# Kernel tuning notes

Hardware: AMD Instinct MI355X
Metric: run time of the kernel (lower is better)

## Reference

```python
import jax, jax.numpy as jnp
from jax import lax
import numpy as np

RANK = 4
C_IN = 32
C_OUT = 64
H, W = 128, 256
L1 = (H + 2, W + 2)      # conv k=3, pad=2, stride=1 -> H+2
L2 = (L1[0] + 2, L1[1] + 2)
EPS = 1e-5


def setup_inputs() -> dict:
    key = jax.random.key(0)
    ks = jax.random.split(key, 12)
    s = lambda k, shp: jax.random.normal(k, shp, dtype=jnp.float32) * 0.05
    inp = {
        "x": jax.random.normal(ks[0], (16, C_IN, H, W), dtype=jnp.float32),
        # layer 1: rank basis kernels, bias, outer combining-weight logits
        "w1": s(ks[1], (RANK, C_OUT, C_IN, 3, 3)),
        "b1": jnp.zeros((C_OUT,), jnp.float32),
        "a1h": s(ks[2], (RANK, L1[0])),
        "a1w": s(ks[3], (RANK, L1[1])),
        "g1": jnp.ones((C_OUT,), jnp.float32),
        "be1": jnp.zeros((C_OUT,), jnp.float32),
        # layer 2
        "w2": s(ks[4], (RANK, C_OUT, C_OUT, 3, 3)),
        "b2": jnp.zeros((C_OUT,), jnp.float32),
        "a2h": s(ks[5], (RANK, L2[0])),
        "a2w": s(ks[6], (RANK, L2[1])),
        "g2": jnp.ones((C_OUT,), jnp.float32),
        "be2": jnp.zeros((C_OUT,), jnp.float32),
    }
    return inp


def _combining_weights(ah, aw):
    # outer sum of row/col logits, softmax over rank -> [rank, Lh, Lw]
    return jax.nn.softmax(ah[:, :, None] + aw[:, None, :], axis=0)


def _lrlc(x, w, b, cw):
    # x: [B, Cin, H, W]; w: [rank, Cout, Cin, 3, 3]; cw: [rank, H', W']
    rank, co, ci, kh, kw = w.shape
    y = lax.conv_general_dilated(
        x, w.reshape(rank * co, ci, kh, kw),
        window_strides=(1, 1), padding=[(2, 2), (2, 2)],
        dimension_numbers=("NCHW", "OIHW", "NCHW"))
    B, _, Ho, Wo = y.shape
    y = y.reshape(B, rank, co, Ho, Wo)
    return jnp.einsum("brohw,rhw->bohw", y, cw) + b[None, :, None, None]


def _bn_relu(x, g, be):
    # training-mode BatchNorm2d (batch stats, biased variance) + ReLU
    mean = jnp.mean(x, axis=(0, 2, 3), keepdims=True)
    var = jnp.var(x, axis=(0, 2, 3), keepdims=True)
    xn = (x - mean) * lax.rsqrt(var + EPS)
    return jax.nn.relu(xn * g[None, :, None, None] + be[None, :, None, None])


def _maxpool3(x):
    return lax.reduce_window(x, -jnp.inf, lax.max,
                             (1, 1, 3, 3), (1, 1, 3, 3), "VALID")


def reference(x, w1, b1, a1h, a1w, g1, be1, w2, b2, a2h, a2w, g2, be2):
    cw1 = _combining_weights(a1h, a1w)
    h = _lrlc(x, w1, b1, cw1)
    h = _bn_relu(h, g1, be1)
    cw2 = _combining_weights(a2h, a2w)
    h = _lrlc(h, w2, b2, cw2)
    h = _bn_relu(h, g2, be2)
    return _maxpool3(h)
```

## Files before the change

kernel.cpp:

```cpp
#include <hip/hip_runtime.h>
#include <hip/hip_bf16.h>
#include <math.h>

#define COUT 64
#define EPS  1e-5f

typedef __hip_bfloat16 bf16;
typedef short  short8  __attribute__((ext_vector_type(8)));
typedef short  short4v __attribute__((ext_vector_type(4)));
typedef float  floatx4 __attribute__((ext_vector_type(4)));

__device__ __forceinline__ short bf16_bits(float f) {
    union { __hip_bfloat16 h; short s; } u;
    u.h = __float2bfloat16(f);
    return u.s;
}
__device__ __forceinline__ float bits_to_f32(short s) {
    union { __hip_bfloat16 h; short s; } u;
    u.s = s;
    return __bfloat162float(u.h);
}

#define NV1   33800
#define NV2   34584
#define XPAD_PLANE  (132*260)
#define H1_PLANE    (134*262)
#define H2_PLANE    (132*260)
#define NPOS1 (16*130*258)
#define NPOS2 (16*132*260)

__global__ void zero_f_kernel(float* __restrict__ p, int n) {
    int i = blockIdx.x*blockDim.x + threadIdx.x;
    if (i < n) p[i] = 0.f;
}
__global__ void zero4_kernel(uint4* __restrict__ p, long n4) {
    long i = (long)blockIdx.x*blockDim.x + threadIdx.x;
    for (; i < n4; i += (long)gridDim.x*blockDim.x) p[i] = make_uint4(0,0,0,0);
}

__global__ void cwv_kernel(const float* __restrict__ ah, const float* __restrict__ aw,
                           float* __restrict__ cwv, int Nv, int Wv, int Lh, int Lw) {
    int idx = blockIdx.x*blockDim.x + threadIdx.x;
    if (idx >= Nv) return;
    int oh = idx / Wv, ow = idx - oh*Wv;
    if (ow > Lw-1) ow = Lw-1;
    float v0 = ah[0*Lh+oh] + aw[0*Lw+ow];
    float v1 = ah[1*Lh+oh] + aw[1*Lw+ow];
    float v2 = ah[2*Lh+oh] + aw[2*Lw+ow];
    float v3 = ah[3*Lh+oh] + aw[3*Lw+ow];
    float m = fmaxf(fmaxf(v0,v1), fmaxf(v2,v3));
    v0 = __expf(v0-m); v1 = __expf(v1-m); v2 = __expf(v2-m); v3 = __expf(v3-m);
    float inv = 1.f/(v0+v1+v2+v3);
    cwv[0*(size_t)Nv+idx] = v0*inv; cwv[1*(size_t)Nv+idx] = v1*inv;
    cwv[2*(size_t)Nv+idx] = v2*inv; cwv[3*(size_t)Nv+idx] = v3*inv;
}

template<int CIN_, int NSLICES>
__global__ void pack_kernel(const float* __restrict__ w, short* __restrict__ Apk) {
    int gid = blockIdx.x*256 + threadIdx.x;
    if (gid >= NSLICES*1024) return;
    int l = gid & 63, t = (gid >> 6) & 15, s = gid >> 10;
    int m = t*16 + (l & 15);
    int r = m >> 6, co = m & 63;
    int kbase = s*32 + ((l >> 4) << 3);
    short8 v;
    #pragma unroll
    for (int j = 0; j < 8; ++j) {
        int k = kbase + j;
        int tap = k / CIN_, ci = k % CIN_;
        float f = w[(((size_t)(r*COUT + co))*CIN_ + ci)*9 + tap];
        v[j] = bf16_bits(f);
    }
    *reinterpret_cast<short8*>(Apk + (size_t)gid*8) = v;
}

__global__ void xpad_kernel(const float* __restrict__ x, short* __restrict__ xp) {
    int row = blockIdx.x;
    int b = row / 132, ih = row - b*132;
    int ci = threadIdx.x & 31, iw0 = threadIdx.x >> 5;
    for (int iw = iw0; iw < 260; iw += 8) {
        float v = 0.f;
        if (ih >= 2 && ih < 130 && iw >= 2 && iw < 258)
            v = x[(((size_t)b*32 + ci)*128 + (ih-2))*256 + (iw-2)];
        xp[((size_t)row*260 + iw)*32 + ci] = bf16_bits(v);
    }
}

template<int CIN_, int NSLICES>
__launch_bounds__(256, 2)
__global__ void lrlc_conv(const short* __restrict__ Bpl, const short* __restrict__ Apk,
                          const float* __restrict__ cwv, const float* __restrict__ bias,
                          short* __restrict__ Out,
                          int Wv, int Hout, int Wreal, int Nv, int inPlanePos,
                          int outW, int outPlanePos, int outPad) {
    const int tid  = threadIdx.x;
    const int w    = tid >> 6, l = tid & 63;
    const int quad = l >> 4, l15 = l & 15;
    const int b    = blockIdx.y;
    const int n0   = blockIdx.x * 64;

    __shared__ float cwS[4*64];
    {
        int r = tid >> 6, nn = tid & 63;
        int n = n0 + nn; if (n > Nv-1) n = Nv-1;
        cwS[r*64 + nn] = cwv[(size_t)r*Nv + n];
    }
    __syncthreads();

    const short* Bb = Bpl + (size_t)b*inPlanePos*CIN_;
    int bOff[4];
    #pragma unroll
    for (int j = 0; j < 4; ++j) bOff[j] = (n0 + j*16 + l15)*CIN_ + quad*8;
    const short* Aw = Apk + (size_t)(w*64 + l)*8;

    floatx4 acc[4][4];
    #pragma unroll
    for (int i = 0; i < 4; ++i)
        #pragma unroll
        for (int j = 0; j < 4; ++j)
            acc[i][j] = (floatx4){0.f,0.f,0.f,0.f};

    for (int s = 0; s < NSLICES; ++s) {
        const int tap = (CIN_ == 32) ? s : (s >> 1);
        const int cb  = (CIN_ == 32) ? 0 : ((s & 1) << 5);
        const int koff = ((tap/3)*Wv + (tap%3))*CIN_ + cb;
        short8 bfr[4], afr[4];
        #pragma unroll
        for (int j = 0; j < 4; ++j)
            bfr[j] = *reinterpret_cast<const short8*>(Bb + bOff[j] + koff);
        #pragma unroll
        for (int i = 0; i < 4; ++i)
            afr[i] = *reinterpret_cast<const short8*>(Aw + (size_t)(s*16 + i*4)*512);
        #pragma unroll
        for (int i = 0; i < 4; ++i)
            #pragma unroll
            for (int j = 0; j < 4; ++j)
                acc[i][j] = __builtin_amdgcn_mfma_f32_16x16x32_bf16(afr[i], bfr[j], acc[i][j], 0, 0, 0);
    }

    const int co_base = w*16 + quad*4;
    float bs[4];
    #pragma unroll
    for (int rg = 0; rg < 4; ++rg) bs[rg] = bias[co_base + rg];
    #pragma unroll
    for (int j = 0; j < 4; ++j) {
        int nl = j*16 + l15;
        int n  = n0 + nl;
        int oh = n / Wv, ow = n - oh*Wv;
        if (ow >= Wreal || oh >= Hout) continue;
        float c0 = cwS[nl], c1 = cwS[64+nl], c2 = cwS[128+nl], c3 = cwS[192+nl];
        short4v pk;
        #pragma unroll
        for (int rg = 0; rg < 4; ++rg) {
            float v = acc[0][j][rg]*c0 + acc[1][j][rg]*c1
                    + acc[2][j][rg]*c2 + acc[3][j][rg]*c3 + bs[rg];
            pk[rg] = bf16_bits(v);
        }
        size_t op = ((size_t)b*outPlanePos + (size_t)(oh + outPad)*outW + (ow + outPad))*(size_t)COUT + co_base;
        *reinterpret_cast<short4v*>(Out + op) = pk;
    }
}

__global__ void stats_nhwc(const short* __restrict__ h, float* __restrict__ sum,
                           float* __restrict__ sq, int npos, int Wreal, int Hreal,
                           int rowW, int planePos, int pad) {
    int c = threadIdx.x & 63, sub = threadIdx.x >> 6;
    float s = 0.f, s2 = 0.f;
    for (long p = blockIdx.x*4 + sub; p < npos; p += (long)gridDim.x*4) {
        int ow = (int)(p % Wreal); long t2 = p / Wreal;
        int oh = (int)(t2 % Hreal); int b = (int)(t2 / Hreal);
        float v = bits_to_f32(h[((size_t)b*planePos + (size_t)(oh+pad)*rowW + ow + pad)*64 + c]);
        s += v; s2 = fmaf(v, v, s2);
    }
    __shared__ float ls[4][64], ls2[4][64];
    ls[sub][c] = s; ls2[sub][c] = s2;
    __syncthreads();
    if (threadIdx.x < 64) {
        float ts  = ls[0][c]+ls[1][c]+ls[2][c]+ls[3][c];
        float ts2 = ls2[0][c]+ls2[1][c]+ls2[2][c]+ls2[3][c];
        atomicAdd(&sum[c], ts);
        atomicAdd(&sq[c], ts2);
    }
}

__global__ void finalize_kernel(const float* __restrict__ sum, const float* __restrict__ sumsq,
                                const float* __restrict__ g, const float* __restrict__ be,
                                float* __restrict__ A, float* __restrict__ Bc, float cnt) {
    int c = threadIdx.x;
    if (c >= COUT) return;
    float mean = sum[c]/cnt;
    float var  = sumsq[c]/cnt - mean*mean;
    float inv  = rsqrtf(var + EPS);
    float a = g[c]*inv;
    A[c]  = a;
    Bc[c] = fmaf(-mean, a, be[c]);
}

__global__ void bnrelu_nhwc(short* __restrict__ h, const float* __restrict__ A,
                            const float* __restrict__ Bc, int npos, int Wreal, int Hreal,
                            int rowW, int planePos, int pad) {
    __shared__ float sA[64], sB[64];
    if (threadIdx.x < 64) { sA[threadIdx.x] = A[threadIdx.x]; sB[threadIdx.x] = Bc[threadIdx.x]; }
    __syncthreads();
    long g = (long)blockIdx.x*256 + threadIdx.x;
    if (g >= (long)npos*16) return;
    int cg = (int)(g & 15); long p = g >> 4;
    int ow = (int)(p % Wreal); long t2 = p / Wreal;
    int oh = (int)(t2 % Hreal); int b = (int)(t2 / Hreal);
    size_t base = ((size_t)b*planePos + (size_t)(oh+pad)*rowW + ow + pad)*64 + cg*4;
    short4v d = *reinterpret_cast<short4v*>(h + base);
    #pragma unroll
    for (int q = 0; q < 4; ++q) {
        float v = bits_to_f32(d[q]);
        int c = cg*4 + q;
        v = fmaxf(fmaf(v, sA[c], sB[c]), 0.f);
        d[q] = bf16_bits(v);
    }
    *reinterpret_cast<short4v*>(h + base) = d;
}

__global__ void maxpool_nhwc(const short* __restrict__ h2, const float* __restrict__ A,
                             const float* __restrict__ Bc, float* __restrict__ out) {
    int idx = blockIdx.x*blockDim.x + threadIdx.x;
    const int total = 16*64*44*86;
    if (idx >= total) return;
    int pw = idx % 86; int t = idx / 86;
    int ph = t % 44;   t /= 44;
    int c  = t % 64;   int b = t / 64;
    float a = A[c], bc = Bc[c];
    float m = 0.f;
    #pragma unroll
    for (int i = 0; i < 3; ++i) {
        size_t rbase = ((size_t)(b*132 + ph*3 + i)*260 + pw*3)*64 + c;
        #pragma unroll
        for (int j = 0; j < 3; ++j) {
            float v = fmaf(bits_to_f32(h2[rbase + (size_t)j*64]), a, bc);
            m = fmaxf(m, v);
        }
    }
    out[idx] = m;
}

extern "C" void kernel_launch(void* const* d_in, const int* in_sizes, int n_in,
                              void* d_out, int out_size, void* d_ws, size_t ws_size,
                              hipStream_t stream) {
    const float* x   = (const float*)d_in[0];
    const float* w1  = (const float*)d_in[1];
    const float* b1  = (const float*)d_in[2];
    const float* a1h = (const float*)d_in[3];
    const float* a1w = (const float*)d_in[4];
    const float* g1  = (const float*)d_in[5];
    const float* be1 = (const float*)d_in[6];
    const float* w2  = (const float*)d_in[7];
    const float* b2  = (const float*)d_in[8];
    const float* a2h = (const float*)d_in[9];
    const float* a2w = (const float*)d_in[10];
    const float* g2  = (const float*)d_in[11];
    const float* be2 = (const float*)d_in[12];
    float* out = (float*)d_out;

    char* ws = (char*)d_ws;
    float* stats = (float*)ws;
    float* sum1 = stats;       float* sq1 = stats + 64;
    float* A1   = stats + 128; float* Bc1 = stats + 192;
    float* sum2 = stats + 256; float* sq2 = stats + 320;
    float* A2   = stats + 384; float* Bc2 = stats + 448;
    float* cw1v = (float*)(ws + 2048);
    float* cw2v = cw1v + 4*NV1;
    short* Apk1 = (short*)(cw2v + 4*NV2);
    short* Apk2 = Apk1 + 73728;
    short* h1pad = Apk2 + 147456;
    short* xpad  = h1pad + (size_t)16*H1_PLANE*64 + 4096;
    short* h2    = xpad;

    zero_f_kernel<<<2, 256, 0, stream>>>(stats, 512);
    {
        long n4 = ((size_t)16*H1_PLANE*64 + 4096) * 2 / 16;
        zero4_kernel<<<4096, 256, 0, stream>>>((uint4*)h1pad, n4);
    }
    cwv_kernel<<<(NV1+255)/256, 256, 0, stream>>>(a1h, a1w, cw1v, NV1, 260, 130, 258);
    cwv_kernel<<<(NV2+255)/256, 256, 0, stream>>>(a2h, a2w, cw2v, NV2, 262, 132, 260);
    pack_kernel<32, 9><<<(9*1024+255)/256, 256, 0, stream>>>(w1, Apk1);
    pack_kernel<64,18><<<(18*1024+255)/256, 256, 0, stream>>>(w2, Apk2);
    xpad_kernel<<<16*132, 256, 0, stream>>>(x, xpad);

    lrlc_conv<32, 9><<<dim3((NV1+63)/64, 16), 256, 0, stream>>>(
        xpad, Apk1, cw1v, b1, h1pad,
        260, 130, 258, NV1, XPAD_PLANE,
        262, H1_PLANE, 2);
    stats_nhwc<<<256, 256, 0, stream>>>(h1pad, sum1, sq1, NPOS1, 258, 130, 262, H1_PLANE, 2);
    finalize_kernel<<<1, 64, 0, stream>>>(sum1, sq1, g1, be1, A1, Bc1, (float)NPOS1);
    bnrelu_nhwc<<<((long)NPOS1*16 + 255)/256, 256, 0, stream>>>(h1pad, A1, Bc1, NPOS1, 258, 130, 262, H1_PLANE, 2);

    lrlc_conv<64,18><<<dim3((NV2+63)/64, 16), 256, 0, stream>>>(
        h1pad, Apk2, cw2v, b2, h2,
        262, 132, 260, NV2, H1_PLANE,
        260, H2_PLANE, 0);
    stats_nhwc<<<256, 256, 0, stream>>>(h2, sum2, sq2, NPOS2, 260, 132, 260, H2_PLANE, 0);
    finalize_kernel<<<1, 64, 0, stream>>>(sum2, sq2, g2, be2, A2, Bc2, (float)NPOS2);

    maxpool_nhwc<<<(16*64*44*86 + 255)/256, 256, 0, stream>>>(h2, A2, Bc2, out);
}
```

Baseline: 1.349 ms.

## Fuse BN stats into conv epilogue, widen conv tile, vectorize bnrelu and maxpool

New measurement: 1.186 ms. -12.1%, faster.

```diff
diff --git a/kernel.cpp b/kernel.cpp
--- a/kernel.cpp
+++ b/kernel.cpp
@@ -68,8 +68,7 @@
     for (int j = 0; j < 8; ++j) {
         int k = kbase + j;
         int tap = k / CIN_, ci = k % CIN_;
-        float f = w[(((size_t)(r*COUT + co))*CIN_ + ci)*9 + tap];
-        v[j] = bf16_bits(f);
+        v[j] = bf16_bits(w[(((size_t)(r*COUT + co))*CIN_ + ci)*9 + tap]);
     }
     *reinterpret_cast<short8*>(Apk + (size_t)gid*8) = v;
 }
@@ -90,43 +89,44 @@
 __launch_bounds__(256, 2)
 __global__ void lrlc_conv(const short* __restrict__ Bpl, const short* __restrict__ Apk,
                           const float* __restrict__ cwv, const float* __restrict__ bias,
-                          short* __restrict__ Out,
+                          short* __restrict__ Out, float* __restrict__ sum, float* __restrict__ sq,
                           int Wv, int Hout, int Wreal, int Nv, int inPlanePos,
                           int outW, int outPlanePos, int outPad) {
     const int tid  = threadIdx.x;
     const int w    = tid >> 6, l = tid & 63;
     const int quad = l >> 4, l15 = l & 15;
     const int b    = blockIdx.y;
-    const int n0   = blockIdx.x * 64;
-
-    __shared__ float cwS[4*64];
-    {
-        int r = tid >> 6, nn = tid & 63;
+    const int n0   = blockIdx.x * 128;
+
+    __shared__ float cwS[4*128];
+    for (int t = tid; t < 512; t += 256) {
+        int r = t >> 7, nn = t & 127;
         int n = n0 + nn; if (n > Nv-1) n = Nv-1;
-        cwS[r*64 + nn] = cwv[(size_t)r*Nv + n];
+        cwS[t] = cwv[(size_t)r*Nv + n];
     }
     __syncthreads();
 
     const short* Bb = Bpl + (size_t)b*inPlanePos*CIN_;
-    int bOff[4];
-    #pragma unroll
-    for (int j = 0; j < 4; ++j) bOff[j] = (n0 + j*16 + l15)*CIN_ + quad*8;
+    int bOff[8];
+    #pragma unroll
+    for (int j = 0; j < 8; ++j) bOff[j] = (n0 + j*16 + l15)*CIN_ + quad*8;
     const short* Aw = Apk + (size_t)(w*64 + l)*8;
 
-    floatx4 acc[4][4];
+    floatx4 acc[4][8];
     #pragma unroll
     for (int i = 0; i < 4; ++i)
         #pragma unroll
-        for (int j = 0; j < 4; ++j)
+        for (int j = 0; j < 8; ++j)
             acc[i][j] = (floatx4){0.f,0.f,0.f,0.f};
 
+    #pragma unroll
     for (int s = 0; s < NSLICES; ++s) {
         const int tap = (CIN_ == 32) ? s : (s >> 1);
         const int cb  = (CIN_ == 32) ? 0 : ((s & 1) << 5);
         const int koff = ((tap/3)*Wv + (tap%3))*CIN_ + cb;
-        short8 bfr[4], afr[4];
-        #pragma unroll
-        for (int j = 0; j < 4; ++j)
+        short8 bfr[8], afr[4];
+        #pragma unroll
+        for (int j = 0; j < 8; ++j)
             bfr[j] = *reinterpret_cast<const short8*>(Bb + bOff[j] + koff);
         #pragma unroll
         for (int i = 0; i < 4; ++i)
@@ -134,7 +134,7 @@
         #pragma unroll
         for (int i = 0; i < 4; ++i)
             #pragma unroll
-            for (int j = 0; j < 4; ++j)
+            for (int j = 0; j < 8; ++j)
                 acc[i][j] = __builtin_amdgcn_mfma_f32_16x16x32_bf16(afr[i], bfr[j], acc[i][j], 0, 0, 0);
     }
 
@@ -142,44 +142,41 @@
     float bs[4];
     #pragma unroll
     for (int rg = 0; rg < 4; ++rg) bs[rg] = bias[co_base + rg];
-    #pragma unroll
-    for (int j = 0; j < 4; ++j) {
+    float st[4] = {0.f,0.f,0.f,0.f}, st2[4] = {0.f,0.f,0.f,0.f};
+    #pragma unroll
+    for (int j = 0; j < 8; ++j) {
         int nl = j*16 + l15;
         int n  = n0 + nl;
         int oh = n / Wv, ow = n - oh*Wv;
-        if (ow >= Wreal || oh >= Hout) continue;
-        float c0 = cwS[nl], c1 = cwS[64+nl], c2 = cwS[128+nl], c3 = cwS[192+nl];
+        bool valid = (ow < Wreal) && (oh < Hout);
+        float c0 = cwS[nl], c1 = cwS[128+nl], c2 = cwS[256+nl], c3 = cwS[384+nl];
         short4v pk;
         #pragma unroll
         for (int rg = 0; rg < 4; ++rg) {
             float v = acc[0][j][rg]*c0 + acc[1][j][rg]*c1
                     + acc[2][j][rg]*c2 + acc[3][j][rg]*c3 + bs[rg];
+            if (valid) { st[rg] += v; st2[rg] = fmaf(v, v, st2[rg]); }
             pk[rg] = bf16_bits(v);
         }
-        size_t op = ((size_t)b*outPlanePos + (size_t)(oh + outPad)*outW + (ow + outPad))*(size_t)COUT + co_base;
-        *reinterpret_cast<short4v*>(Out + op) = pk;
-    }
-}
-
-__global__ void stats_nhwc(const short* __restrict__ h, float* __restrict__ sum,
-                           float* __restrict__ sq, int npos, int Wreal, int Hreal,
-                           int rowW, int planePos, int pad) {
-    int c = threadIdx.x & 63, sub = threadIdx.x >> 6;
-    float s = 0.f, s2 = 0.f;
-    for (long p = blockIdx.x*4 + sub; p < npos; p += (long)gridDim.x*4) {
-        int ow = (int)(p % Wreal); long t2 = p / Wreal;
-        int oh = (int)(t2 % Hreal); int b = (int)(t2 / Hreal);
-        float v = bits_to_f32(h[((size_t)b*planePos + (size_t)(oh+pad)*rowW + ow + pad)*64 + c]);
-        s += v; s2 = fmaf(v, v, s2);
-    }
-    __shared__ float ls[4][64], ls2[4][64];
-    ls[sub][c] = s; ls2[sub][c] = s2;
-    __syncthreads();
-    if (threadIdx.x < 64) {
-        float ts  = ls[0][c]+ls[1][c]+ls[2][c]+ls[3][c];
-        float ts2 = ls2[0][c]+ls2[1][c]+ls2[2][c]+ls2[3][c];
-        atomicAdd(&sum[c], ts);
-        atomicAdd(&sq[c], ts2);
+        if (valid) {
+            size_t op = ((size_t)b*outPlanePos + (size_t)(oh + outPad)*outW + (ow + outPad))*(size_t)COUT + co_base;
+            *reinterpret_cast<short4v*>(Out + op) = pk;
+        }
+    }
+    #pragma unroll
+    for (int m = 1; m < 16; m <<= 1) {
+        #pragma unroll
+        for (int rg = 0; rg < 4; ++rg) {
+            st[rg]  += __shfl_xor(st[rg],  m, 16);
+            st2[rg] += __shfl_xor(st2[rg], m, 16);
+        }
+    }
+    if (l15 == 0) {
+        #pragma unroll
+        for (int rg = 0; rg < 4; ++rg) {
+            atomicAdd(&sum[co_base+rg], st[rg]);
+            atomicAdd(&sq[co_base+rg],  st2[rg]);
+        }
     }
 }
 
@@ -196,49 +193,57 @@
     Bc[c] = fmaf(-mean, a, be[c]);
 }
 
-__global__ void bnrelu_nhwc(short* __restrict__ h, const float* __restrict__ A,
-                            const float* __restrict__ Bc, int npos, int Wreal, int Hreal,
-                            int rowW, int planePos, int pad) {
+__global__ void bnrelu_rows(short* __restrict__ h, const float* __restrict__ A,
+                            const float* __restrict__ Bc) {
     __shared__ float sA[64], sB[64];
     if (threadIdx.x < 64) { sA[threadIdx.x] = A[threadIdx.x]; sB[threadIdx.x] = Bc[threadIdx.x]; }
     __syncthreads();
-    long g = (long)blockIdx.x*256 + threadIdx.x;
-    if (g >= (long)npos*16) return;
-    int cg = (int)(g & 15); long p = g >> 4;
-    int ow = (int)(p % Wreal); long t2 = p / Wreal;
-    int oh = (int)(t2 % Hreal); int b = (int)(t2 / Hreal);
-    size_t base = ((size_t)b*planePos + (size_t)(oh+pad)*rowW + ow + pad)*64 + cg*4;
-    short4v d = *reinterpret_cast<short4v*>(h + base);
-    #pragma unroll
-    for (int q = 0; q < 4; ++q) {
-        float v = bits_to_f32(d[q]);
-        int c = cg*4 + q;
-        v = fmaxf(fmaf(v, sA[c], sB[c]), 0.f);
-        d[q] = bf16_bits(v);
-    }
-    *reinterpret_cast<short4v*>(h + base) = d;
-}
-
-__global__ void maxpool_nhwc(const short* __restrict__ h2, const float* __restrict__ A,
+    int row = blockIdx.x;
+    int b = row / 130, oh = row - b*130;
+    short* base = h + ((size_t)(b*134 + oh + 2)*262 + 2)*64;
+    const int nvec = 258*64/8;
+    for (int it = threadIdx.x; it < nvec; it += 256) {
+        short8 d = *reinterpret_cast<short8*>(base + it*8);
+        int c0 = (it*8) & 63;
+        #pragma unroll
+        for (int q = 0; q < 8; ++q) {
+            float v = bits_to_f32(d[q]);
+            int c = c0 + q;
+            v = fmaxf(fmaf(v, sA[c], sB[c]), 0.f);
+            d[q] = bf16_bits(v);
+        }
+        *reinterpret_cast<short8*>(base + it*8) = d;
+    }
+}
+
+__global__ void maxpool_rows(const short* __restrict__ h2, const float* __restrict__ A,
                              const float* __restrict__ Bc, float* __restrict__ out) {
-    int idx = blockIdx.x*blockDim.x + threadIdx.x;
-    const int total = 16*64*44*86;
-    if (idx >= total) return;
-    int pw = idx % 86; int t = idx / 86;
-    int ph = t % 44;   t /= 44;
-    int c  = t % 64;   int b = t / 64;
-    float a = A[c], bc = Bc[c];
-    float m = 0.f;
-    #pragma unroll
-    for (int i = 0; i < 3; ++i) {
-        size_t rbase = ((size_t)(b*132 + ph*3 + i)*260 + pw*3)*64 + c;
-        #pragma unroll
-        for (int j = 0; j < 3; ++j) {
-            float v = fmaf(bits_to_f32(h2[rbase + (size_t)j*64]), a, bc);
-            m = fmaxf(m, v);
-        }
-    }
-    out[idx] = m;
+    __shared__ float sA[64], sB[64];
+    if (threadIdx.x < 64) { sA[threadIdx.x] = A[threadIdx.x]; sB[threadIdx.x] = Bc[threadIdx.x]; }
+    __syncthreads();
+    int row = blockIdx.x;
+    int b = row / 44, ph = row - b*44;
+    for (int item = threadIdx.x; item < 86*16; item += 256) {
+        int cg = item & 15, pw = item >> 4;
+        float m[4] = {0.f,0.f,0.f,0.f};
+        #pragma unroll
+        for (int i = 0; i < 3; ++i) {
+            const short* rp = h2 + ((size_t)(b*132 + ph*3 + i)*260 + pw*3)*64 + cg*4;
+            #pragma unroll
+            for (int j = 0; j < 3; ++j) {
+                short4v d = *reinterpret_cast<const short4v*>(rp + j*64);
+                #pragma unroll
+                for (int q = 0; q < 4; ++q) {
+                    int c = cg*4 + q;
+                    float v = fmaf(bits_to_f32(d[q]), sA[c], sB[c]);
+                    m[q] = fmaxf(m[q], v);
+                }
+            }
+        }
+        #pragma unroll
+        for (int q = 0; q < 4; ++q)
+            out[((size_t)(b*64 + cg*4 + q)*44 + ph)*86 + pw] = m[q];
+    }
 }
 
 extern "C" void kernel_launch(void* const* d_in, const int* in_sizes, int n_in,
@@ -284,20 +289,16 @@
     pack_kernel<64,18><<<(18*1024+255)/256, 256, 0, stream>>>(w2, Apk2);
     xpad_kernel<<<16*132, 256, 0, stream>>>(x, xpad);
 
-    lrlc_conv<32, 9><<<dim3((NV1+63)/64, 16), 256, 0, stream>>>(
-        xpad, Apk1, cw1v, b1, h1pad,
-        260, 130, 258, NV1, XPAD_PLANE,
-        262, H1_PLANE, 2);
-    stats_nhwc<<<256, 256, 0, stream>>>(h1pad, sum1, sq1, NPOS1, 258, 130, 262, H1_PLANE, 2);
+    lrlc_conv<32, 9><<<dim3((NV1+127)/128, 16), 256, 0, stream>>>(
+        xpad, Apk1, cw1v, b1, h1pad, sum1, sq1,
+        260, 130, 258, NV1, XPAD_PLANE, 262, H1_PLANE, 2);
     finalize_kernel<<<1, 64, 0, stream>>>(sum1, sq1, g1, be1, A1, Bc1, (float)NPOS1);
-    bnrelu_nhwc<<<((long)NPOS1*16 + 255)/256, 256, 0, stream>>>(h1pad, A1, Bc1, NPOS1, 258, 130, 262, H1_PLANE, 2);
-
-    lrlc_conv<64,18><<<dim3((NV2+63)/64, 16), 256, 0, stream>>>(
-        h1pad, Apk2, cw2v, b2, h2,
-        262, 132, 260, NV2, H1_PLANE,
-        260, H2_PLANE, 0);
-    stats_nhwc<<<256, 256, 0, stream>>>(h2, sum2, sq2, NPOS2, 260, 132, 260, H2_PLANE, 0);
+    bnrelu_rows<<<16*130, 256, 0, stream>>>(h1pad, A1, Bc1);
+
+    lrlc_conv<64,18><<<dim3((NV2+127)/128, 16), 256, 0, stream>>>(
+        h1pad, Apk2, cw2v, b2, h2, sum2, sq2,
+        262, 132, 260, NV2, H1_PLANE, 260, H2_PLANE, 0);
     finalize_kernel<<<1, 64, 0, stream>>>(sum2, sq2, g2, be2, A2, Bc2, (float)NPOS2);
 
-    maxpool_nhwc<<<(16*64*44*86 + 255)/256, 256, 0, stream>>>(h2, A2, Bc2, out);
-}
+    maxpool_rows<<<16*44, 256, 0, stream>>>(h2, A2, Bc2, out);
+}
```
